# Kernel tuning notes

Measured on AMD Instinct MI355X. Metric: run time of the kernel, lower is better.

The kernel has to match this reference:

```python
import jax, jax.numpy as jnp
from jax import lax
import numpy as np

SEQ_LEN = 2048
BATCH = 512
HIDDEN = 256
CLASSES = 10


def setup_inputs() -> dict:
    key = jax.random.key(0)
    k1, k2, k3, k4 = jax.random.split(key, 4)
    return {
        "x": jax.random.normal(k1, (BATCH, SEQ_LEN), dtype=jnp.float32),
        "W_hx": jax.random.normal(k2, (HIDDEN, 1), dtype=jnp.float32),
        "W_hh": jax.random.normal(k3, (HIDDEN, HIDDEN), dtype=jnp.float32),
        "W_ph": jax.random.normal(k4, (CLASSES, HIDDEN), dtype=jnp.float32),
        "bias_h": jnp.zeros((HIDDEN, 1), dtype=jnp.float32),
        "bias_p": jnp.zeros((CLASSES,), dtype=jnp.float32),
    }


def reference(x, W_hx, W_hh, W_ph, bias_h, bias_p):
    # x: [B, T]. Hidden state h: [H, B]. Only last-step p is returned,
    # matching the torch loop where p is overwritten each iteration.
    B = x.shape[0]
    h0 = jnp.zeros((W_hh.shape[0], B), dtype=x.dtype)

    def step(h, x_t):  # x_t: [B]
        # W_hx @ x_t[None,:] : [H,1]@[1,B] -> [H,B]
        h_new = jnp.tanh(W_hx @ x_t[None, :] + W_hh @ h + bias_h)
        return h_new, None

    h_T, _ = lax.scan(step, h0, x.T)  # scan over time: x.T is [T, B]
    p = h_T.T @ W_ph.T + bias_p  # [B, C]
    return p
```

## Files before the change

### kernel.cpp

```cpp
#include <hip/hip_runtime.h>
#include <math.h>


#define TT 2048
#define BB 512
#define HH 256
#define CC 10
#define KH 128

__device__ __forceinline__ float ref_tanhf(float x)
{
    const float a1  = 4.89352455891786e-03f;
    const float a3  = 6.37261928875436e-04f;
    const float a5  = 1.48572235717979e-05f;
    const float a7  = 5.12229709037114e-08f;
    const float a9  = -8.60467152213735e-11f;
    const float a11 = 2.00018790482477e-13f;
    const float a13 = -2.76076847742355e-16f;
    const float b0  = 4.89352518554385e-03f;
    const float b2  = 2.26843463243900e-03f;
    const float b4  = 1.18534705686654e-04f;
    const float b6  = 1.19825839466702e-06f;

    const float kClamp = 7.99881172180175781f;
    const float xc = fmaxf(fminf(x, kClamp), -kClamp);
    const float x2 = __fmul_rn(xc, xc);
    float p = fmaf(x2, a13, a11);
    p = fmaf(x2, p, a9);
    p = fmaf(x2, p, a7);
    p = fmaf(x2, p, a5);
    p = fmaf(x2, p, a3);
    p = fmaf(x2, p, a1);
    p = __fmul_rn(xc, p);
    float q = fmaf(x2, b6, b4);
    q = fmaf(x2, q, b2);
    q = fmaf(x2, q, b0);
    const float r = __fdiv_rn(p, q);
    return (fabsf(x) < 0.0004f) ? x : r;
}

__global__ __launch_bounds__(512, 1)
void rnn_fwd(const float* __restrict__ x,
             const float* __restrict__ W_hx,
             const float* __restrict__ W_hh,
             const float* __restrict__ W_ph,
             const float* __restrict__ bias_h,
             const float* __restrict__ bias_p,
             float* __restrict__ out)
{
    const int tid   = threadIdx.x;
    const int group = tid >> 8;
    const int i     = tid & (HH - 1);
    const int b0    = blockIdx.x * 2;

    __shared__ __align__(16) float xls[2][TT];
    __shared__ __align__(16) float hbuf[2][2][HH];
    __shared__ __align__(16) float zpart[2][HH];

    float w[KH];
    const float* __restrict__ wrow = W_hh + (size_t)i * HH + group * KH;
#pragma unroll
    for (int k = 0; k < KH; k += 4) {
        const float4 v = *reinterpret_cast<const float4*>(wrow + k);
        w[k] = v.x; w[k + 1] = v.y; w[k + 2] = v.z; w[k + 3] = v.w;
    }
#pragma unroll
    for (int k = 0; k < KH; ++k) {
        asm volatile("" : "+v"(w[k]));
    }

    {
        const float4* __restrict__ xsrc =
            reinterpret_cast<const float4*>(x + (size_t)b0 * TT);
        float4* __restrict__ xdst = reinterpret_cast<float4*>(&xls[0][0]);
        xdst[tid]       = xsrc[tid];
        xdst[512 + tid] = xsrc[512 + tid];
    }
    const float whx = W_hx[i];
    const float bh  = bias_h[i];

    hbuf[group][1][i] = 0.0f;
    __syncthreads();

#define PBODY(COL, T, RP)                                                     \
    {                                                                         \
        const float* __restrict__ h = &hbuf[(COL)][(RP)][0];                  \
        float z = 0.0f;                                                       \
        _Pragma("unroll")                                                     \
        for (int k = 0; k < KH; k += 4) {                                     \
            const float4 h4 = *reinterpret_cast<const float4*>(h + k);        \
            z = fmaf(w[k],     h4.x, z);                                      \
            z = fmaf(w[k + 1], h4.y, z);                                      \
            z = fmaf(w[k + 2], h4.z, z);                                      \
            z = fmaf(w[k + 3], h4.w, z);                                      \
        }                                                                     \
        zpart[(COL)][i] = z;                                                  \
    }

#define QBODY(COL, T, RP)                                                     \
    {                                                                         \
        const float* __restrict__ h = &hbuf[(COL)][(RP)][0];                  \
        float z = zpart[(COL)][i];                                            \
        _Pragma("unroll")                                                     \
        for (int k = 0; k < KH; k += 4) {                                     \
            const float4 h4 = *reinterpret_cast<const float4*>(h + KH + k);   \
            z = fmaf(w[k],     h4.x, z);                                      \
            z = fmaf(w[k + 1], h4.y, z);                                      \
            z = fmaf(w[k + 2], h4.z, z);                                      \
            z = fmaf(w[k + 3], h4.w, z);                                      \
        }                                                                     \
        const float a0 = __fmul_rn(whx, xls[(COL)][(T)]);                     \
        z = __fadd_rn(__fadd_rn(a0, z), bh);                                  \
        hbuf[(COL)][(RP) ^ 1][i] = ref_tanhf(z);                              \
    }

#define STEP(U, RP)                                                           \
    {                                                                         \
        if (group == 0) { PBODY(0, (U), (RP)) }                               \
        else if ((U) >= 1) { QBODY(1, (U) - 1, (RP) ^ 1) }                    \
        __syncthreads();                                                      \
        if (group == 0) { PBODY(1, (U), (RP)) }                               \
        else { QBODY(0, (U), (RP)) }                                          \
        __syncthreads();                                                      \
    }

    STEP(0, 1)
    for (int u = 1; u + 1 < TT; u += 2) {
        STEP(u, 0)
        STEP(u + 1, 1)
    }
    STEP(TT - 1, 0)
    if (group == 1) { QBODY(1, TT - 1, 0) }
    __syncthreads();

#undef STEP
#undef QBODY
#undef PBODY

    if (tid < 2 * CC) {
        const int col = tid / CC;
        const int c   = tid % CC;
        const float* __restrict__ wp = W_ph + (size_t)c * HH;
        const float* __restrict__ hf = hbuf[col][1];
        float pv = 0.0f;
#pragma unroll 8
        for (int k = 0; k < HH; ++k) {
            pv = fmaf(hf[k], wp[k], pv);
        }
        out[(size_t)(b0 + col) * CC + c] = __fadd_rn(pv, bias_p[c]);
    }
}

extern "C" void kernel_launch(void* const* d_in, const int* in_sizes, int n_in,
                              void* d_out, int out_size, void* d_ws, size_t ws_size,
                              hipStream_t stream) {
    const float* x      = (const float*)d_in[0];
    const float* W_hx   = (const float*)d_in[1];
    const float* W_hh   = (const float*)d_in[2];
    const float* W_ph   = (const float*)d_in[3];
    const float* bias_h = (const float*)d_in[4];
    const float* bias_p = (const float*)d_in[5];
    float* out = (float*)d_out;

    rnn_fwd<<<dim3(BB / 2), dim3(512), 0, stream>>>(x, W_hx, W_hh, W_ph, bias_h, bias_p, out);
}
```

Measured before the change: 3.073 ms.

## Halve block size and give each thread two hidden rows of W_hh

The block shrinks from 512 to 256 threads, and each thread now holds two 128-element weight row segments (256 VGPRs) instead of one. Each LDS float4 load of h is reused across two independent FMA chains. This halves LDS broadcast traffic and gives more instruction-level parallelism per thread, at the cost of doubling per-thread work per step and nearly exhausting the register budget. The risk is register spills or a longer per-step critical path that the fewer waves cannot hide.

After: 8.176 ms. 2.66x slower.

```diff
diff --git a/kernel.cpp b/kernel.cpp
--- a/kernel.cpp
+++ b/kernel.cpp
@@ -39,7 +39,7 @@
     return (fabsf(x) < 0.0004f) ? x : r;
 }
 
-__global__ __launch_bounds__(512, 1)
+__global__ __launch_bounds__(256, 1)
 void rnn_fwd(const float* __restrict__ x,
              const float* __restrict__ W_hx,
              const float* __restrict__ W_hh,
@@ -49,69 +49,84 @@
              float* __restrict__ out)
 {
     const int tid   = threadIdx.x;
-    const int group = tid >> 8;
-    const int i     = tid & (HH - 1);
+    const int group = tid >> 7;
+    const int r     = tid & 127;
     const int b0    = blockIdx.x * 2;
 
     __shared__ __align__(16) float xls[2][TT];
     __shared__ __align__(16) float hbuf[2][2][HH];
     __shared__ __align__(16) float zpart[2][HH];
 
-    float w[KH];
-    const float* __restrict__ wrow = W_hh + (size_t)i * HH + group * KH;
+    float wa[KH], wb[KH];
+    {
+        const float* __restrict__ wra = W_hh + (size_t)r * HH + group * KH;
+        const float* __restrict__ wrb = W_hh + (size_t)(r + 128) * HH + group * KH;
 #pragma unroll
-    for (int k = 0; k < KH; k += 4) {
-        const float4 v = *reinterpret_cast<const float4*>(wrow + k);
-        w[k] = v.x; w[k + 1] = v.y; w[k + 2] = v.z; w[k + 3] = v.w;
+        for (int k = 0; k < KH; k += 4) {
+            const float4 va = *reinterpret_cast<const float4*>(wra + k);
+            wa[k] = va.x; wa[k + 1] = va.y; wa[k + 2] = va.z; wa[k + 3] = va.w;
+            const float4 vb = *reinterpret_cast<const float4*>(wrb + k);
+            wb[k] = vb.x; wb[k + 1] = vb.y; wb[k + 2] = vb.z; wb[k + 3] = vb.w;
+        }
     }
 #pragma unroll
     for (int k = 0; k < KH; ++k) {
-        asm volatile("" : "+v"(w[k]));
+        asm volatile("" : "+v"(wa[k]));
+        asm volatile("" : "+v"(wb[k]));
     }
 
     {
         const float4* __restrict__ xsrc =
             reinterpret_cast<const float4*>(x + (size_t)b0 * TT);
         float4* __restrict__ xdst = reinterpret_cast<float4*>(&xls[0][0]);
-        xdst[tid]       = xsrc[tid];
-        xdst[512 + tid] = xsrc[512 + tid];
+#pragma unroll
+        for (int j = 0; j < 4; ++j) {
+            xdst[j * 256 + tid] = xsrc[j * 256 + tid];
+        }
     }
-    const float whx = W_hx[i];
-    const float bh  = bias_h[i];
+    const float whxa = W_hx[r];
+    const float whxb = W_hx[r + 128];
+    const float bha  = bias_h[r];
+    const float bhb  = bias_h[r + 128];
 
-    hbuf[group][1][i] = 0.0f;
+    hbuf[0][1][tid] = 0.0f;
+    hbuf[1][1][tid] = 0.0f;
     __syncthreads();
+
+#define CHAIN4(H4, K)                                                         \
+    za = fmaf(wa[(K)],     H4.x, za);  zv = fmaf(wb[(K)],     H4.x, zv);      \
+    za = fmaf(wa[(K) + 1], H4.y, za);  zv = fmaf(wb[(K) + 1], H4.y, zv);      \
+    za = fmaf(wa[(K) + 2], H4.z, za);  zv = fmaf(wb[(K) + 2], H4.z, zv);      \
+    za = fmaf(wa[(K) + 3], H4.w, za);  zv = fmaf(wb[(K) + 3], H4.w, zv);
 
 #define PBODY(COL, T, RP)                                                     \
     {                                                                         \
         const float* __restrict__ h = &hbuf[(COL)][(RP)][0];                  \
-        float z = 0.0f;                                                       \
+        float za = 0.0f, zv = 0.0f;                                           \
         _Pragma("unroll")                                                     \
-        for (int k = 0; k < KH; k += 4) {                                     \
-            const float4 h4 = *reinterpret_cast<const float4*>(h + k);        \
-            z = fmaf(w[k],     h4.x, z);                                      \
-            z = fmaf(w[k + 1], h4.y, z);                                      \
-            z = fmaf(w[k + 2], h4.z, z);                                      \
-            z = fmaf(w[k + 3], h4.w, z);                                      \
+        for (int j = 0; j < KH; j += 4) {                                     \
+            const float4 h4 = *reinterpret_cast<const float4*>(h + j);        \
+            CHAIN4(h4, j)                                                     \
         }                                                                     \
-        zpart[(COL)][i] = z;                                                  \
+        zpart[(COL)][r] = za;  zpart[(COL)][r + 128] = zv;                    \
     }
 
 #define QBODY(COL, T, RP)                                                     \
     {                                                                         \
-        const float* __restrict__ h = &hbuf[(COL)][(RP)][0];                  \
-        float z = zpart[(COL)][i];                                            \
+        const float* __restrict__ h = &hbuf[(COL)][(RP)][KH];                 \
+        float za = zpart[(COL)][r], zv = zpart[(COL)][r + 128];               \
         _Pragma("unroll")                                                     \
-        for (int k = 0; k < KH; k += 4) {                                     \
-            const float4 h4 = *reinterpret_cast<const float4*>(h + KH + k);   \
-            z = fmaf(w[k],     h4.x, z);                                      \
-            z = fmaf(w[k + 1], h4.y, z);                                      \
-            z = fmaf(w[k + 2], h4.z, z);                                      \
-            z = fmaf(w[k + 3], h4.w, z);                                      \
+        for (int j = 0; j < KH; j += 4) {                                     \
+            const float4 h4 = *reinterpret_cast<const float4*>(h + j);        \
+            CHAIN4(h4, j)                                                     \
         }                                                                     \
-        const float a0 = __fmul_rn(whx, xls[(COL)][(T)]);                     \
-        z = __fadd_rn(__fadd_rn(a0, z), bh);                                  \
-        hbuf[(COL)][(RP) ^ 1][i] = ref_tanhf(z);                              \
+        const float xt = xls[(COL)][(T)];                                     \
+        const float aa = __fmul_rn(whxa, xt);                                 \
+        const float ab = __fmul_rn(whxb, xt);                                 \
+        za = __fadd_rn(__fadd_rn(aa, za), bha);                               \
+        zv = __fadd_rn(__fadd_rn(ab, zv), bhb);                               \
+        hbuf[(COL)][(RP) ^ 1][r]       = ref_tanhf(za);                       \
+        hbuf[(COL)][(RP) ^ 1][r + 128] = ref_tanhf(zv);                       \
     }
 
 #define STEP(U, RP)                                                           \
@@ -136,6 +151,7 @@
 #undef STEP
 #undef QBODY
 #undef PBODY
+#undef CHAIN4
 
     if (tid < 2 * CC) {
         const int col = tid / CC;
@@ -162,5 +178,5 @@
     const float* bias_p = (const float*)d_in[5];
     float* out = (float*)d_out;
 
-    rnn_fwd<<<dim3(BB / 2), dim3(512), 0, stream>>>(x, W_hx, W_hh, W_ph, bias_h, bias_p, out);
+    rnn_fwd<<<dim3(BB / 2), dim3(256), 0, stream>>>(x, W_hx, W_hh, W_ph, bias_h, bias_p, out);
 }
```
